# Performance work log

Hardware: AMD Instinct MI355X
Metric: run time of the kernel (lower is better)

The kernel has to match this reference:

```python
import jax, jax.numpy as jnp
import numpy as np

BL = 512  # block length (matches init bl)


def _conv1x1(w, b, x):
    # w: (out, in), b: (out,), x: (batch, in, L) -> (batch, out, L)
    return jnp.einsum('oi,bil->bol', w, x) + b[None, :, None]


def _window_mask(bl):
    # Faithful to torch loop: window_mask[:, :, i:i+bl] = 1 for i in range(bl)
    # -> all ones except the last column.
    wm = np.zeros((1, bl, bl + 2 * (bl // 2)), np.float32)
    for i in range(bl):
        wm[:, :, i:i + bl] = 1.0
    return jnp.asarray(wm)


def setup_inputs() -> dict:
    key = jax.random.key(0)
    ks = jax.random.split(key, 5)
    B, C, L = 1, 2048, 16384
    Cq = C // 2  # r1 = r2 = r3 = 2
    s_in = 1.0 / float(np.sqrt(C))
    s_mid = 1.0 / float(np.sqrt(Cq))
    return {
        'x1': jax.random.normal(ks[0], (B, C, L), jnp.float32),
        'x2': jnp.zeros((B, C, L), jnp.float32),
        'mask': jnp.ones((B, 1, L), jnp.float32),
        'wq': jax.random.normal(ks[1], (Cq, C), jnp.float32) * s_in,
        'bq': jnp.zeros((Cq,), jnp.float32),
        'wk': jax.random.normal(ks[2], (Cq, C), jnp.float32) * s_in,
        'bk': jnp.zeros((Cq,), jnp.float32),
        'wv': jax.random.normal(ks[3], (Cq, C), jnp.float32) * s_in,
        'bv': jnp.zeros((Cq,), jnp.float32),
        'wo': jax.random.normal(ks[4], (C, Cq), jnp.float32) * s_mid,
        'bo': jnp.zeros((C,), jnp.float32),
    }


def reference(x1, x2, mask, wq, bq, wk, bk, wv, bv, wo, bo):
    B, C, L = x1.shape  # B == 1 (asserted by sliding path)
    bl = BL
    nb = L // bl  # L % bl == 0 by construction
    half = bl // 2

    q = _conv1x1(wq, bq, x1)  # (1, c, L)
    k = _conv1x1(wk, bk, x1)
    v = _conv1x1(wv, bv, x1)  # encoder stage: value from x1 (x2 unused)
    c = q.shape[1]

    # query blocks: (nb, c, bl)
    qb = q.reshape(B, c, nb, bl).transpose(0, 2, 1, 3).reshape(nb, c, bl)

    # pad k/v/padding_mask with bl//2 zeros on both sides, then take overlapping
    # windows of width 2*bl per block.
    kp = jnp.pad(k, ((0, 0), (0, 0), (half, half)))[0]            # (c, L+bl)
    vp = jnp.pad(v, ((0, 0), (0, 0), (half, half)))[0]
    pm = jnp.pad(mask[:, 0:1, :], ((0, 0), (0, 0), (half, half)))[0]  # (1, L+bl)
    cols = np.arange(nb)[:, None] * bl + np.arange(2 * bl)[None, :]   # (nb, 2bl)
    kb = kp[:, cols].transpose(1, 0, 2)   # (nb, c, 2bl)
    vb = vp[:, cols].transpose(1, 0, 2)   # (nb, c, 2bl)
    pmb = pm[:, cols].transpose(1, 0, 2)  # (nb, 1, 2bl)

    final_mask = _window_mask(bl) * pmb   # (nb, bl, 2bl)

    # scalar dot attention with log-mask (as in AttentionHelper.scalar_dot_att)
    energy = jnp.einsum('ncl,ncm->nlm', qb, kb) / jnp.float32(np.sqrt(c))
    attn = jax.nn.softmax(energy + jnp.log(final_mask + 1e-9), axis=-1)
    attn = attn * final_mask
    out = jnp.einsum('ncm,nlm->ncl', vb, attn)  # (nb, c, bl)

    out = _conv1x1(wo, bo, jax.nn.relu(out))    # (nb, C, bl)
    out = out.reshape(B, nb, C, bl).transpose(0, 2, 1, 3).reshape(B, C, nb * bl)
    out = out[:, :, :L]
    return out * mask[:, 0:1, :]
```

## Files before the change

kernel.cpp:

```cpp
#include <hip/hip_runtime.h>
#include <hip/hip_bf16.h>

typedef __attribute__((ext_vector_type(4))) float f32x4;
typedef __attribute__((ext_vector_type(8))) __bf16 bf16x8;

#define DEVINL static __device__ __forceinline__

DEVINL unsigned short f2bf(float f) {
  union { float f; unsigned u; } x; x.f = f;
  return (unsigned short)((x.u + 0x7FFFu + ((x.u >> 16) & 1u)) >> 16);
}

DEVINL void gload16(const void* g, void* l) {
  __builtin_amdgcn_global_load_lds((const __attribute__((address_space(1))) void*)g,
                                   (__attribute__((address_space(3))) void*)l,
                                   16, 0, 0);
}

#define SBAR()   asm volatile("s_barrier" ::: "memory")
#define LGKM0()  asm volatile("s_waitcnt lgkmcnt(0)" ::: "memory")
#define VM(n)    asm volatile("s_waitcnt vmcnt(" #n ")" ::: "memory")

__global__ __launch_bounds__(256) void transpose_x_k(const float* __restrict__ x,
                                                     unsigned short* __restrict__ xT) {
  __shared__ float tile[32][33];
  const int bx = blockIdx.x;
  const int by = blockIdx.y;
  const int tx = threadIdx.x;
  const int ty = threadIdx.y;
#pragma unroll
  for (int i = 0; i < 4; ++i) {
    int c = by * 32 + ty + i * 8;
    tile[ty + i * 8][tx] = x[(long)c * 16384 + bx * 32 + tx];
  }
  __syncthreads();
#pragma unroll
  for (int i = 0; i < 4; ++i) {
    int l = bx * 32 + ty + i * 8;
    xT[(long)l * 2048 + by * 32 + tx] = f2bf(tile[tx][ty + i * 8]);
  }
}

__global__ __launch_bounds__(256) void conv_w_k(const float* __restrict__ wq,
                                                const float* __restrict__ wk,
                                                const float* __restrict__ wv,
                                                const float* __restrict__ wo,
                                                unsigned short* __restrict__ Wqk,
                                                unsigned short* __restrict__ Wv,
                                                unsigned short* __restrict__ Wo) {
  long i = (long)blockIdx.x * 256 + threadIdx.x;
  if (i < 4194304) {
    float s = (i < 2097152) ? wq[i] : wk[i - 2097152];
    Wqk[i] = f2bf(s);
  } else if (i < 6291456) {
    Wv[i - 4194304] = f2bf(wv[i - 4194304]);
  } else {
    Wo[i - 6291456] = f2bf(wo[i - 6291456]);
  }
}

enum { EPI_QK = 0, EPI_V = 1, EPI_S = 2, EPI_PV = 3, EPI_OUT = 4 };

struct GArgs {
  const unsigned short* A;
  const unsigned short* Bt;
  void* C;
  const float* bias;
  const float* bias2;
  const float* mask;
  const unsigned short* guard;
  int aBatch, cBatch;
  int btRow0, btRow0Step, btRowLim;
  int btK0, btK0Step, btKLim;
};

template <int EPI, int GUARDED, int LDA, int LDB, int LDC, int KK>
__global__ __launch_bounds__(512, 2) void gemm8_k(GArgs g) {
  constexpr int NK = KK >> 6;
  constexpr int NT = NK >> 1;
  __shared__ char lds[131072];

  const int t = threadIdx.x;
  const int l = t & 63;
  const int w = t >> 6;

  const int gx = gridDim.x, gxy = gx * gridDim.y;
  const int nwg = gxy * gridDim.z;
  int lin = blockIdx.z * gxy + blockIdx.y * gx + blockIdx.x;
  lin = (lin & 7) * (nwg >> 3) + (lin >> 3);
  const int z = lin / gxy;
  const int rres = lin - z * gxy;
  const int Mbase = (rres / gx) << 8;
  const int Nbase = (rres - (rres / gx) * gx) << 8;

  const int wr = w >> 2;
  const int wc = w & 3;
  const int fr = l & 15;
  const int fg = l >> 4;

  const unsigned short* Ab = g.A + (long)z * g.aBatch + (long)Mbase * LDA;
  const int bRowBase = g.btRow0 + z * g.btRow0Step + Nbase;
  const int bK0 = g.btK0 + z * g.btK0Step;

  const int rr = t >> 3;
  const int cb8s = t & 7;

  auto stage = [&](int bufSel, int unit, int kt) {
    const int k0 = (kt & (NK - 1)) << 6;
    const bool isA = (unit == 0) || (unit == 3);
#pragma unroll
    for (int gph = 0; gph < 2; ++gph) {
      int row;
      if (isA) row = (unit == 0 ? 0 : 64) + (gph << 7) + rr;
      else     row = (unit == 1 ? 0 : 32) + (gph << 7) + (rr & 31) + ((rr >> 5) << 6);
      const int cbL = cb8s ^ (row & 7);
      const int gk = k0 + (cbL << 3);
      char* lp = lds + (bufSel << 16) + (isA ? 0 : 32768) + row * 128 + (cb8s << 4);
      const char* gp;
      if (isA) {
        gp = (const char*)(Ab + (long)row * LDA + gk);
      } else if (!GUARDED) {
        gp = (const char*)(g.Bt + (long)(bRowBase + row) * LDB + (bK0 + gk));
      } else {
        const int grow = bRowBase + row;
        const int gkk = bK0 + gk;
        if ((unsigned)grow < (unsigned)g.btRowLim && (unsigned)gkk < (unsigned)g.btKLim)
          gp = (const char*)(g.Bt + (long)grow * LDB + gkk);
        else
          gp = (const char*)g.guard + (l << 4);
      }
      gload16(gp, lp);
    }
  };

  const int arow = (wr << 7) + fr;
  const int brow = (wc << 6) + fr;

  auto ldA = [&](int i8, int kk, int bufSel) -> bf16x8 {
    const int row = arow + (i8 << 4);
    const int cb = ((kk << 2) | fg) ^ (row & 7);
    return *(const bf16x8*)(lds + (bufSel << 16) + row * 128 + (cb << 4));
  };
  auto ldB = [&](int j, int kk, int bufSel) -> bf16x8 {
    const int row = brow + (j << 4);
    const int cb = ((kk << 2) | fg) ^ (row & 7);
    return *(const bf16x8*)(lds + (bufSel << 16) + 32768 + row * 128 + (cb << 4));
  };

  f32x4 acc[8][4];
#pragma unroll
  for (int i = 0; i < 8; ++i)
#pragma unroll
    for (int j = 0; j < 4; ++j) acc[i][j] = f32x4{0.f, 0.f, 0.f, 0.f};

  stage(0, 0, 0); stage(0, 1, 0); stage(0, 2, 0); stage(0, 3, 0);
  stage(1, 0, 1); stage(1, 1, 1); stage(1, 2, 1);
  VM(6);
  SBAR();

  bf16x8 fa[4][2], fb[4][2];

#define MFMA_Q(QI, QJ)                                                        \
  __builtin_amdgcn_s_setprio(1);                                              \
  _Pragma("unroll") for (int i = 0; i < 4; ++i)                               \
  _Pragma("unroll") for (int j = 0; j < 2; ++j)                               \
  _Pragma("unroll") for (int kk = 0; kk < 2; ++kk)                            \
    acc[(QI)*4 + i][(QJ)*2 + j] = __builtin_amdgcn_mfma_f32_16x16x32_bf16(    \
        fa[i][kk], fb[(QJ)*2 + j][kk], acc[(QI)*4 + i][(QJ)*2 + j], 0, 0, 0); \
  __builtin_amdgcn_s_setprio(0);

#pragma unroll 1
  for (int it = 0; it < NT; ++it) {
    const int kt1 = 2 * it + 1;
    const int ktn0 = 2 * it + 2;
    const int ktn1 = 2 * it + 3;
#pragma unroll
    for (int i = 0; i < 4; ++i) { fa[i][0] = ldA(i, 0, 0); fa[i][1] = ldA(i, 1, 0); }
#pragma unroll
    for (int j = 0; j < 2; ++j) { fb[j][0] = ldB(j, 0, 0); fb[j][1] = ldB(j, 1, 0); }
    stage(1, 3, kt1);
    SBAR(); LGKM0();
    MFMA_Q(0, 0);
    SBAR();
#pragma unroll
    for (int j = 2; j < 4; ++j) { fb[j][0] = ldB(j, 0, 0); fb[j][1] = ldB(j, 1, 0); }
    stage(0, 0, ktn0);
    SBAR(); LGKM0();
    MFMA_Q(0, 1);
    SBAR();
#pragma unroll
    for (int i = 0; i < 4; ++i) { fa[i][0] = ldA(4 + i, 0, 0); fa[i][1] = ldA(4 + i, 1, 0); }
    stage(0, 1, ktn0);
    SBAR(); LGKM0();
    MFMA_Q(1, 0);
    SBAR();
    stage(0, 2, ktn0);
    SBAR(); LGKM0();
    MFMA_Q(1, 1);
    VM(6);
    SBAR();
#pragma unroll
    for (int i = 0; i < 4; ++i) { fa[i][0] = ldA(i, 0, 1); fa[i][1] = ldA(i, 1, 1); }
#pragma unroll
    for (int j = 0; j < 2; ++j) { fb[j][0] = ldB(j, 0, 1); fb[j][1] = ldB(j, 1, 1); }
    stage(0, 3, ktn0);
    SBAR(); LGKM0();
    MFMA_Q(0, 0);
    SBAR();
#pragma unroll
    for (int j = 2; j < 4; ++j) { fb[j][0] = ldB(j, 0, 1); fb[j][1] = ldB(j, 1, 1); }
    stage(1, 0, ktn1);
    SBAR(); LGKM0();
    MFMA_Q(0, 1);
    SBAR();
#pragma unroll
    for (int i = 0; i < 4; ++i) { fa[i][0] = ldA(4 + i, 0, 1); fa[i][1] = ldA(4 + i, 1, 1); }
    stage(1, 1, ktn1);
    SBAR(); LGKM0();
    MFMA_Q(1, 0);
    SBAR();
    stage(1, 2, ktn1);
    SBAR(); LGKM0();
    MFMA_Q(1, 1);
    VM(6);
    SBAR();
  }
  VM(0); LGKM0(); SBAR();

#pragma unroll
  for (int ii = 0; ii < 8; ++ii)
#pragma unroll
    for (int j = 0; j < 4; ++j)
#pragma unroll
      for (int r = 0; r < 4; ++r) {
        const int row = Mbase + (wr << 7) + ii * 16 + fg * 4 + r;
        const int col = Nbase + (wc << 6) + j * 16 + fr;
        float val = acc[ii][j][r];
        const long off = (long)z * g.cBatch + (long)row * LDC + col;
        if (EPI == EPI_QK) {
          val = (col < 1024) ? (val + g.bias[col]) * 0.03125f
                             : (val + g.bias2[col - 1024]);
          ((unsigned short*)g.C)[off] = f2bf(val);
        } else if (EPI == EPI_V) {
          val += g.bias[row];
          ((unsigned short*)g.C)[off] = f2bf(val);
        } else if (EPI == EPI_S) {
          ((float*)g.C)[off] = val;
        } else if (EPI == EPI_PV) {
          val = fmaxf(val, 0.f);
          ((unsigned short*)g.C)[off] = f2bf(val);
        } else {
          val = (val + g.bias[row]) * g.mask[col];
          ((float*)g.C)[off] = val;
        }
      }
#undef MFMA_Q
}

__global__ __launch_bounds__(256) void softmax_k(const float* __restrict__ S,
                                                 const float* __restrict__ mask,
                                                 unsigned short* __restrict__ P) {
  const int row = blockIdx.x;
  const int n = row >> 9;
  const float* s = S + (long)row * 1024;
  unsigned short* p = P + (long)row * 1024;
  const int t = threadIdx.x;

  float logit[4], fm[4];
  float lmax = -3.0e38f;
#pragma unroll
  for (int i = 0; i < 4; ++i) {
    int m = i * 256 + t;
    int pos = (n << 9) + m - 256;
    float f = (((unsigned)pos < 16384u) && (m != 1023)) ? mask[pos] : 0.f;
    float lg = s[m] + logf(f + 1e-9f);
    fm[i] = f; logit[i] = lg;
    lmax = fmaxf(lmax, lg);
  }
#pragma unroll
  for (int o = 32; o; o >>= 1) lmax = fmaxf(lmax, __shfl_xor(lmax, o, 64));
  __shared__ float red[8];
  const int wv_ = t >> 6, ln = t & 63;
  if (ln == 0) red[wv_] = lmax;
  __syncthreads();
  const float gmax = fmaxf(fmaxf(red[0], red[1]), fmaxf(red[2], red[3]));

  float e[4], lsum = 0.f;
#pragma unroll
  for (int i = 0; i < 4; ++i) { e[i] = expf(logit[i] - gmax); lsum += e[i]; }
#pragma unroll
  for (int o = 32; o; o >>= 1) lsum += __shfl_xor(lsum, o, 64);
  __syncthreads();
  if (ln == 0) red[4 + wv_] = lsum;
  __syncthreads();
  const float inv = 1.f / ((red[4] + red[5]) + (red[6] + red[7]));
#pragma unroll
  for (int i = 0; i < 4; ++i) {
    int m = i * 256 + t;
    p[m] = f2bf(e[i] * inv * fm[i]);
  }
}

extern "C" void kernel_launch(void* const* d_in, const int* in_sizes, int n_in,
                              void* d_out, int out_size, void* d_ws, size_t ws_size,
                              hipStream_t stream) {
  const float* x1 = (const float*)d_in[0];
  const float* mask = (const float*)d_in[2];
  const float* wq = (const float*)d_in[3];
  const float* bq = (const float*)d_in[4];
  const float* wk = (const float*)d_in[5];
  const float* bk = (const float*)d_in[6];
  const float* wv = (const float*)d_in[7];
  const float* bv = (const float*)d_in[8];
  const float* wo = (const float*)d_in[9];
  const float* bo = (const float*)d_in[10];

  char* ws = (char*)d_ws;
  unsigned short* xT   = (unsigned short*)(ws);
  unsigned short* attT = xT;
  unsigned short* Wqk  = (unsigned short*)(ws + 67108864);
  unsigned short* Wv   = (unsigned short*)(ws + 75497472);
  unsigned short* Wo   = (unsigned short*)(ws + 79691776);
  unsigned short* qkT  = (unsigned short*)(ws + 83886080);
  unsigned short* vbuf = (unsigned short*)(ws + 150994944);
  float*          Sbuf = (float*)(ws + 184549376);
  unsigned short* P    = (unsigned short*)(ws + 251658240);
  unsigned short* guard= (unsigned short*)(ws + 285212672);

  hipMemsetAsync(guard, 0, 4096, stream);

  transpose_x_k<<<dim3(512, 64), dim3(32, 8), 0, stream>>>(x1, xT);
  conv_w_k<<<dim3(32768), dim3(256), 0, stream>>>(wq, wk, wv, wo, Wqk, Wv, Wo);

  const int BIG = 0x40000000;
  {
    GArgs a{};
    a.A = xT; a.Bt = Wqk; a.C = qkT;
    a.bias = bq; a.bias2 = bk; a.guard = guard;
    a.aBatch = 0; a.cBatch = 0;
    a.btRow0 = 0; a.btRow0Step = 0; a.btRowLim = BIG;
    a.btK0 = 0; a.btK0Step = 0; a.btKLim = BIG;
    gemm8_k<EPI_QK, 0, 2048, 2048, 2048, 2048><<<dim3(8, 64, 1), 512, 0, stream>>>(a);
  }
  {
    GArgs a{};
    a.A = Wv; a.Bt = xT; a.C = vbuf;
    a.bias = bv; a.guard = guard;
    a.aBatch = 0; a.cBatch = 0;
    a.btRow0 = 0; a.btRow0Step = 0; a.btRowLim = BIG;
    a.btK0 = 0; a.btK0Step = 0; a.btKLim = BIG;
    gemm8_k<EPI_V, 0, 2048, 2048, 16384, 2048><<<dim3(64, 4, 1), 512, 0, stream>>>(a);
  }
  {
    GArgs a{};
    a.A = qkT; a.Bt = qkT; a.C = Sbuf;
    a.guard = guard;
    a.aBatch = 512 * 2048; a.cBatch = 512 * 1024;
    a.btRow0 = -256; a.btRow0Step = 512; a.btRowLim = 16384;
    a.btK0 = 1024; a.btK0Step = 0; a.btKLim = BIG;
    gemm8_k<EPI_S, 1, 2048, 2048, 1024, 1024><<<dim3(4, 2, 32), 512, 0, stream>>>(a);
  }
  softmax_k<<<dim3(16384), dim3(256), 0, stream>>>(Sbuf, mask, P);
  {
    GArgs a{};
    a.A = P; a.Bt = vbuf; a.C = attT;
    a.guard = guard;
    a.aBatch = 512 * 1024; a.cBatch = 512 * 1024;
    a.btRow0 = 0; a.btRow0Step = 0; a.btRowLim = BIG;
    a.btK0 = -256; a.btK0Step = 512; a.btKLim = 16384;
    gemm8_k<EPI_PV, 1, 1024, 16384, 1024, 1024><<<dim3(4, 2, 32), 512, 0, stream>>>(a);
  }
  {
    GArgs a{};
    a.A = Wo; a.Bt = attT; a.C = d_out;
    a.bias = bo; a.mask = mask; a.guard = guard;
    a.aBatch = 0; a.cBatch = 0;
    a.btRow0 = 0; a.btRow0Step = 0; a.btRowLim = BIG;
    a.btK0 = 0; a.btK0Step = 0; a.btKLim = BIG;
    gemm8_k<EPI_OUT, 0, 1024, 1024, 16384, 1024><<<dim3(64, 8, 1), 512, 0, stream>>>(a);
  }
  (void)in_sizes; (void)n_in; (void)out_size; (void)ws_size;
}
```

Before: 469.3 us.

## Vectorize transpose, weight conversion and softmax I/O; reorder MFMA loop and add partial waits

Each thread in the x transpose, the weight bf16 conversion and the softmax now handles four consecutive elements, using float4 loads and 8-byte packed bf16 stores in place of scalar accesses. The weight-conversion grid shrinks to match. In softmax, one redundant __syncthreads is removed and the mask/column indexing switches to a contiguous per-thread layout. In the GEMM, the MFMA inner loop is reordered to put kk outermost, and an lgkmcnt(8) wait is inserted before the barrier. These target memory-transaction count and some sync overhead in the helper kernels, while the main GEMM changes are small scheduling tweaks that could shift instruction interleaving.

```diff
diff --git a/kernel.cpp b/kernel.cpp
--- a/kernel.cpp
+++ b/kernel.cpp
@@ -3,6 +3,8 @@
 
 typedef __attribute__((ext_vector_type(4))) float f32x4;
 typedef __attribute__((ext_vector_type(8))) __bf16 bf16x8;
+
+struct ushort4_t { unsigned short x, y, z, w; };
 
 #define DEVINL static __device__ __forceinline__
 
@@ -19,6 +21,7 @@
 
 #define SBAR()   asm volatile("s_barrier" ::: "memory")
 #define LGKM0()  asm volatile("s_waitcnt lgkmcnt(0)" ::: "memory")
+#define LGKM8()  asm volatile("s_waitcnt lgkmcnt(8)" ::: "memory")
 #define VM(n)    asm volatile("s_waitcnt vmcnt(" #n ")" ::: "memory")
 
 __global__ __launch_bounds__(256) void transpose_x_k(const float* __restrict__ x,
@@ -34,11 +37,15 @@
     tile[ty + i * 8][tx] = x[(long)c * 16384 + bx * 32 + tx];
   }
   __syncthreads();
-#pragma unroll
-  for (int i = 0; i < 4; ++i) {
-    int l = bx * 32 + ty + i * 8;
-    xT[(long)l * 2048 + by * 32 + tx] = f2bf(tile[tx][ty + i * 8]);
-  }
+  const int t = ty * 32 + tx;
+  const int lrow = t >> 3;
+  const int cq = (t & 7) << 2;
+  ushort4_t o;
+  o.x = f2bf(tile[cq + 0][lrow]);
+  o.y = f2bf(tile[cq + 1][lrow]);
+  o.z = f2bf(tile[cq + 2][lrow]);
+  o.w = f2bf(tile[cq + 3][lrow]);
+  *reinterpret_cast<ushort4_t*>(xT + (long)(bx * 32 + lrow) * 2048 + by * 32 + cq) = o;
 }
 
 __global__ __launch_bounds__(256) void conv_w_k(const float* __restrict__ wq,
@@ -48,15 +55,22 @@
                                                 unsigned short* __restrict__ Wqk,
                                                 unsigned short* __restrict__ Wv,
                                                 unsigned short* __restrict__ Wo) {
-  long i = (long)blockIdx.x * 256 + threadIdx.x;
+  long i = ((long)blockIdx.x * 256 + threadIdx.x) * 4;
+  const float* src;
+  unsigned short* dst;
   if (i < 4194304) {
-    float s = (i < 2097152) ? wq[i] : wk[i - 2097152];
-    Wqk[i] = f2bf(s);
+    src = (i < 2097152) ? (wq + i) : (wk + i - 2097152);
+    dst = Wqk + i;
   } else if (i < 6291456) {
-    Wv[i - 4194304] = f2bf(wv[i - 4194304]);
+    src = wv + (i - 4194304);
+    dst = Wv + (i - 4194304);
   } else {
-    Wo[i - 6291456] = f2bf(wo[i - 6291456]);
-  }
+    src = wo + (i - 6291456);
+    dst = Wo + (i - 6291456);
+  }
+  float4 v = *reinterpret_cast<const float4*>(src);
+  ushort4_t o{f2bf(v.x), f2bf(v.y), f2bf(v.z), f2bf(v.w)};
+  *reinterpret_cast<ushort4_t*>(dst) = o;
 }
 
 enum { EPI_QK = 0, EPI_V = 1, EPI_S = 2, EPI_PV = 3, EPI_OUT = 4 };
@@ -162,9 +176,9 @@
 
 #define MFMA_Q(QI, QJ)                                                        \
   __builtin_amdgcn_s_setprio(1);                                              \
+  _Pragma("unroll") for (int kk = 0; kk < 2; ++kk)                            \
   _Pragma("unroll") for (int i = 0; i < 4; ++i)                               \
   _Pragma("unroll") for (int j = 0; j < 2; ++j)                               \
-  _Pragma("unroll") for (int kk = 0; kk < 2; ++kk)                            \
     acc[(QI)*4 + i][(QJ)*2 + j] = __builtin_amdgcn_mfma_f32_16x16x32_bf16(    \
         fa[i][kk], fb[(QJ)*2 + j][kk], acc[(QI)*4 + i][(QJ)*2 + j], 0, 0, 0); \
   __builtin_amdgcn_s_setprio(0);
@@ -179,6 +193,7 @@
 #pragma unroll
     for (int j = 0; j < 2; ++j) { fb[j][0] = ldB(j, 0, 0); fb[j][1] = ldB(j, 1, 0); }
     stage(1, 3, kt1);
+    LGKM8();
     SBAR(); LGKM0();
     MFMA_Q(0, 0);
     SBAR();
@@ -204,6 +219,7 @@
 #pragma unroll
     for (int j = 0; j < 2; ++j) { fb[j][0] = ldB(j, 0, 1); fb[j][1] = ldB(j, 1, 1); }
     stage(0, 3, ktn0);
+    LGKM8();
     SBAR(); LGKM0();
     MFMA_Q(0, 0);
     SBAR();
@@ -266,16 +282,20 @@
   unsigned short* p = P + (long)row * 1024;
   const int t = threadIdx.x;
 
-  float logit[4], fm[4];
+  const float4 sv = *reinterpret_cast<const float4*>(s + t * 4);
+  const int pos0 = (n << 9) + t * 4 - 256;
+  float4 mv = {0.f, 0.f, 0.f, 0.f};
+  if ((unsigned)pos0 < 16384u) mv = *reinterpret_cast<const float4*>(mask + pos0);
+  float fm[4] = {mv.x, mv.y, mv.z, mv.w};
+  if (t == 255) fm[3] = 0.f;
+  const float sc[4] = {sv.x, sv.y, sv.z, sv.w};
+
+  float logit[4];
   float lmax = -3.0e38f;
 #pragma unroll
-  for (int i = 0; i < 4; ++i) {
-    int m = i * 256 + t;
-    int pos = (n << 9) + m - 256;
-    float f = (((unsigned)pos < 16384u) && (m != 1023)) ? mask[pos] : 0.f;
-    float lg = s[m] + logf(f + 1e-9f);
-    fm[i] = f; logit[i] = lg;
-    lmax = fmaxf(lmax, lg);
+  for (int k = 0; k < 4; ++k) {
+    logit[k] = sc[k] + logf(fm[k] + 1e-9f);
+    lmax = fmaxf(lmax, logit[k]);
   }
 #pragma unroll
   for (int o = 32; o; o >>= 1) lmax = fmaxf(lmax, __shfl_xor(lmax, o, 64));
@@ -287,18 +307,18 @@
 
   float e[4], lsum = 0.f;
 #pragma unroll
-  for (int i = 0; i < 4; ++i) { e[i] = expf(logit[i] - gmax); lsum += e[i]; }
+  for (int k = 0; k < 4; ++k) { e[k] = expf(logit[k] - gmax); lsum += e[k]; }
 #pragma unroll
   for (int o = 32; o; o >>= 1) lsum += __shfl_xor(lsum, o, 64);
-  __syncthreads();
   if (ln == 0) red[4 + wv_] = lsum;
   __syncthreads();
   const float inv = 1.f / ((red[4] + red[5]) + (red[6] + red[7]));
-#pragma unroll
-  for (int i = 0; i < 4; ++i) {
-    int m = i * 256 + t;
-    p[m] = f2bf(e[i] * inv * fm[i]);
-  }
+  ushort4_t o4;
+  o4.x = f2bf(e[0] * inv * fm[0]);
+  o4.y = f2bf(e[1] * inv * fm[1]);
+  o4.z = f2bf(e[2] * inv * fm[2]);
+  o4.w = f2bf(e[3] * inv * fm[3]);
+  *reinterpret_cast<ushort4_t*>(p + t * 4) = o4;
 }
 
 extern "C" void kernel_launch(void* const* d_in, const int* in_sizes, int n_in,
@@ -330,7 +350,7 @@
   hipMemsetAsync(guard, 0, 4096, stream);
 
   transpose_x_k<<<dim3(512, 64), dim3(32, 8), 0, stream>>>(x1, xT);
-  conv_w_k<<<dim3(32768), dim3(256), 0, stream>>>(wq, wk, wv, wo, Wqk, Wv, Wo);
+  conv_w_k<<<dim3(8192), dim3(256), 0, stream>>>(wq, wk, wv, wo, Wqk, Wv, Wo);
 
   const int BIG = 0x40000000;
   {
```

After: 464.0 us. Within noise of the previous version (-1.1%).
